# Kernel optimization log

Hardware: AMD Instinct MI355X
Metric: run time of the kernel (lower is better)

The kernel has to match this reference:

```python
import jax, jax.numpy as jnp
import numpy as np

B, LC, LP = 8, 1024, 512
D, H, F, V, NL = 512, 8, 2048, 70, 4
MAXLEN = 2048
HD = D // H
EPS = 1e-5


def setup_inputs() -> dict:
    key = jax.random.key(0)
    ks = iter(jax.random.split(key, 64))
    s = lambda *sh: jax.random.normal(next(ks), sh, jnp.float32) * 0.02
    inp = {}
    inp['cds'] = jax.random.randint(next(ks), (B, LC), 0, V)
    inp['enc_prot'] = jax.random.normal(next(ks), (B, LP, D), jnp.float32)
    causal = jnp.tril(jnp.ones((LC, LC), jnp.int32))
    inp['cds_mask'] = jnp.broadcast_to(causal[None, None], (B, 1, LC, LC))
    inp['prot_mask'] = jnp.ones((B, 1, 1, LP), jnp.int32)
    inp['tok_emb'] = s(V, D)
    inp['pos_emb'] = s(MAXLEN, D)
    for p in ['sa', 'ca']:
        for m in ['q', 'k', 'v', 'o']:
            inp[f'{p}_w{m}'] = s(NL, D, D)
            inp[f'{p}_b{m}'] = jnp.zeros((NL, D), jnp.float32)
    inp['ff_w1'] = s(NL, D, F)
    inp['ff_b1'] = jnp.zeros((NL, F), jnp.float32)
    inp['ff_w2'] = s(NL, F, D)
    inp['ff_b2'] = jnp.zeros((NL, D), jnp.float32)
    for i in [1, 2, 3]:
        inp[f'ln{i}_g'] = jnp.ones((NL, D), jnp.float32)
        inp[f'ln{i}_b'] = jnp.zeros((NL, D), jnp.float32)
    inp['fc_out_w'] = s(D, V)
    inp['fc_out_b'] = jnp.zeros((V,), jnp.float32)
    return inp


def layernorm(x, g, b):
    mu = jnp.mean(x, -1, keepdims=True)
    var = jnp.var(x, -1, keepdims=True)
    return (x - mu) * jax.lax.rsqrt(var + EPS) * g + b


def mha(q_in, k_in, v_in, wq, bq, wk, bk, wv, bv, wo, bo, mask):
    b, lq, _ = q_in.shape
    lk = k_in.shape[1]
    q = (q_in @ wq + bq).reshape(b, lq, H, HD).transpose(0, 2, 1, 3)
    k = (k_in @ wk + bk).reshape(b, lk, H, HD).transpose(0, 2, 1, 3)
    v = (v_in @ wv + bv).reshape(b, lk, H, HD).transpose(0, 2, 1, 3)
    scores = jnp.einsum('bhqd,bhkd->bhqk', q, k) / jnp.sqrt(jnp.float32(HD))
    scores = jnp.where(mask == 0, -jnp.inf, scores)
    attn = jax.nn.softmax(scores, axis=-1)
    out = jnp.einsum('bhqk,bhkd->bhqd', attn, v)
    out = out.transpose(0, 2, 1, 3).reshape(b, lq, D)
    return out @ wo + bo, attn


def reference(cds, enc_prot, cds_mask, prot_mask, tok_emb, pos_emb,
              sa_wq, sa_bq, sa_wk, sa_bk, sa_wv, sa_bv, sa_wo, sa_bo,
              ca_wq, ca_bq, ca_wk, ca_bk, ca_wv, ca_bv, ca_wo, ca_bo,
              ff_w1, ff_b1, ff_w2, ff_b2,
              ln1_g, ln1_b, ln2_g, ln2_b, ln3_g, ln3_b,
              fc_out_w, fc_out_b):
    lc = cds.shape[1]
    x = tok_emb[cds] * jnp.sqrt(jnp.float32(D)) + pos_emb[:lc][None]
    attn = None
    for i in range(NL):
        sa, _ = mha(x, x, x, sa_wq[i], sa_bq[i], sa_wk[i], sa_bk[i],
                    sa_wv[i], sa_bv[i], sa_wo[i], sa_bo[i], cds_mask)
        x = layernorm(x + sa, ln1_g[i], ln1_b[i])
        ca, attn = mha(x, enc_prot, enc_prot, ca_wq[i], ca_bq[i], ca_wk[i], ca_bk[i],
                       ca_wv[i], ca_bv[i], ca_wo[i], ca_bo[i], prot_mask)
        x = layernorm(x + ca, ln2_g[i], ln2_b[i])
        ff = jax.nn.relu(x @ ff_w1[i] + ff_b1[i]) @ ff_w2[i] + ff_b2[i]
        x = layernorm(x + ff, ln3_g[i], ln3_b[i])
    logits = x @ fc_out_w + fc_out_b
    return logits, attn
```

## Files before the change

### kernel.cpp

```cpp
#include <hip/hip_runtime.h>

typedef __attribute__((ext_vector_type(8))) short bf16x8;
typedef __attribute__((ext_vector_type(4))) short bf16x4;
typedef __attribute__((ext_vector_type(2))) short bf16x2;
typedef __attribute__((ext_vector_type(4))) float f32x4;

#define D_MODEL 512
#define N_HEADS 8
#define HEAD_DIM 64
#define SEQ_C 1024
#define SEQ_P 512
#define BATCH 8
#define FFDIM 2048
#define VOCAB 70
#define NLAYER 4
#define MQ (BATCH*SEQ_C)
#define MKV (BATCH*SEQ_P)
#define KSTR 72

__device__ __forceinline__ short f2bs(float f) {
  union { float f; unsigned u; } v; v.f = f;
  unsigned r = (v.u + 0x7FFFu + ((v.u >> 16) & 1u)) >> 16;
  return (short)r;
}

__device__ __forceinline__ void gl_lds16(const void* g, void* l) {
  __builtin_amdgcn_global_load_lds(
      (const __attribute__((address_space(1))) void*)g,
      (__attribute__((address_space(3))) void*)l, 16, 0, 0);
}

__global__ __launch_bounds__(256)
void embed_kernel(const int* __restrict__ cds, const float* __restrict__ tok,
                  const float* __restrict__ pos, float* __restrict__ x,
                  short* __restrict__ xb) {
  int idx = blockIdx.x * 256 + threadIdx.x;
  int row = idx >> 9, c = idx & 511;
  int l = row & (SEQ_C - 1);
  int t = cds[row];
  float v = tok[t * D_MODEL + c] * 22.627416997969522f + pos[l * D_MODEL + c];
  x[idx] = v;
  xb[idx] = f2bs(v);
}

__global__ __launch_bounds__(256)
void cvtf2b_kernel(const float* __restrict__ in, short* __restrict__ out) {
  int i = (blockIdx.x * 256 + threadIdx.x) * 4;
  float4 v = *(const float4*)(in + i);
  bf16x4 o;
  o[0] = f2bs(v.x); o[1] = f2bs(v.y); o[2] = f2bs(v.z); o[3] = f2bs(v.w);
  *(bf16x4*)(out + i) = o;
}

struct WtArgs {
  const float* src[8];
  short* dst[8];
  size_t ldz[8];
  int row_off[8];
};

__global__ __launch_bounds__(256)
void wtrans8_kernel(WtArgs a) {
  __shared__ float T[32][33];
  int z = blockIdx.z;
  int job = z >> 2, layer = z & 3;
  const float* W = a.src[job] + (size_t)layer * D_MODEL * D_MODEL;
  short* Wt = a.dst[job] + (size_t)layer * a.ldz[job];
  int row_off = a.row_off[job];
  int n0 = blockIdx.x * 32, k0 = blockIdx.y * 32;
  int r = threadIdx.x >> 3, c4 = (threadIdx.x & 7) * 4;
  float4 v = *(const float4*)(W + (size_t)(k0 + r) * D_MODEL + n0 + c4);
  T[c4 + 0][r] = v.x; T[c4 + 1][r] = v.y; T[c4 + 2][r] = v.z; T[c4 + 3][r] = v.w;
  __syncthreads();
  bf16x4 o;
  o[0] = f2bs(T[r][c4 + 0]); o[1] = f2bs(T[r][c4 + 1]);
  o[2] = f2bs(T[r][c4 + 2]); o[3] = f2bs(T[r][c4 + 3]);
  *(bf16x4*)&Wt[(size_t)(row_off + n0 + r) * D_MODEL + k0 + c4] = o;
}

__global__ __launch_bounds__(256)
void wtrans_kernel(const float* __restrict__ W, short* __restrict__ Wt,
                   int K, int N, size_t dst_ldz) {
  __shared__ float T[32][33];
  size_t lo_s = (size_t)blockIdx.z * K * N;
  size_t lo_d = (size_t)blockIdx.z * dst_ldz;
  int n0 = blockIdx.x * 32, k0 = blockIdx.y * 32;
  int r = threadIdx.x >> 3, c4 = (threadIdx.x & 7) * 4;
  float4 v = *(const float4*)(W + lo_s + (size_t)(k0 + r) * N + n0 + c4);
  T[c4 + 0][r] = v.x; T[c4 + 1][r] = v.y; T[c4 + 2][r] = v.z; T[c4 + 3][r] = v.w;
  __syncthreads();
  bf16x4 o;
  o[0] = f2bs(T[r][c4 + 0]); o[1] = f2bs(T[r][c4 + 1]);
  o[2] = f2bs(T[r][c4 + 2]); o[3] = f2bs(T[r][c4 + 3]);
  *(bf16x4*)&Wt[lo_d + (size_t)(n0 + r) * K + k0 + c4] = o;
}

__global__ __launch_bounds__(256)
void logits_wt_kernel(const float* __restrict__ w, short* __restrict__ wt) {
  int idx = blockIdx.x * 256 + threadIdx.x;
  int r = idx >> 9, c = idx & 511;
  wt[idx] = (r < VOCAB) ? f2bs(w[c * VOCAB + r]) : (short)0;
}

template<int ACT, int OMODE, int MT>
__global__ __launch_bounds__(256)
void gemm_mfma(const short* __restrict__ Ab, const short* __restrict__ Wt,
               const float* __restrict__ b0, const float* __restrict__ b1,
               const float* __restrict__ b2,
               float* __restrict__ Cf, short* __restrict__ Cb,
               int N, int K, int ldc, size_t segstride) {
  constexpr int MREP = MT / 32;
  __shared__ __align__(16) short As[2][MT * 32];
  __shared__ __align__(16) short Bs[2][4096];
  int tid = threadIdx.x, lane = tid & 63, w = tid >> 6;
  int quad = lane >> 4, ln = lane & 15;
  int row0 = blockIdx.x * MT, col0 = blockIdx.y * 128;
  int q0 = tid, q1 = tid + 256;
  const short* a0 = Ab + (size_t)(row0 + (q0 >> 2)) * K + (q0 & 3) * 8;
  const short* a1 = Ab + (size_t)(row0 + (q1 >> 2)) * K + (q1 & 3) * 8;
  const short* w0 = Wt + (size_t)(col0 + (q0 >> 2)) * K + (q0 & 3) * 8;
  const short* w1 = Wt + (size_t)(col0 + (q1 >> 2)) * K + (q1 & 3) * 8;
  int wr = (w >> 1) * (MT / 2), wc = (w & 1) * 64;
  f32x4 acc[MREP][4];
  #pragma unroll
  for (int mb = 0; mb < MREP; mb++)
    #pragma unroll
    for (int nb = 0; nb < 4; nb++) acc[mb][nb] = (f32x4){0.f, 0.f, 0.f, 0.f};

  int nt = K >> 5;
#define STG(ko, buf) do { \
    gl_lds16(a0 + (ko), &As[buf][w * 512]); \
    if (MT == 128) gl_lds16(a1 + (ko), &As[buf][MT * 16 + w * 512]); \
    gl_lds16(w0 + (ko), &Bs[buf][w * 512]); \
    gl_lds16(w1 + (ko), &Bs[buf][2048 + w * 512]); } while (0)

  STG(0, 0);
  __syncthreads();
  for (int t = 0; t < nt; t++) {
    int cur = t & 1;
    if (t + 1 < nt) STG((t + 1) << 5, cur ^ 1);
    bf16x8 af[MREP], bfr[4];
    #pragma unroll
    for (int i = 0; i < MREP; i++)
      af[i] = *(const bf16x8*)&As[cur][(wr + i * 16 + ln) * 32 + quad * 8];
    #pragma unroll
    for (int i = 0; i < 4; i++)
      bfr[i] = *(const bf16x8*)&Bs[cur][(wc + i * 16 + ln) * 32 + quad * 8];
    #pragma unroll
    for (int mb = 0; mb < MREP; mb++)
      #pragma unroll
      for (int nb = 0; nb < 4; nb++)
        acc[mb][nb] = __builtin_amdgcn_mfma_f32_16x16x32_bf16(
            af[mb], bfr[nb], acc[mb][nb], 0, 0, 0);
    __syncthreads();
  }
#undef STG

  int colb = col0 + wc;
  const float* bp = b0;
  if (OMODE == 2) {
    int seg = colb >> 9;
    bp = (seg == 0) ? b0 : (seg == 1) ? b1 : b2;
  }
  float bv[4];
  #pragma unroll
  for (int nb = 0; nb < 4; nb++) {
    int col = colb + nb * 16 + ln;
    if (OMODE == 3)      bv[nb] = (col < ldc) ? bp[col] : 0.f;
    else if (OMODE == 2) bv[nb] = bp[col & 511];
    else                 bv[nb] = bp[col];
  }
  size_t segoff = (OMODE == 2) ? (size_t)(colb >> 9) * segstride : 0;
  #pragma unroll
  for (int mb = 0; mb < MREP; mb++)
    #pragma unroll
    for (int i = 0; i < 4; i++) {
      size_t r = (size_t)(row0 + wr + mb * 16 + quad * 4 + i);
      #pragma unroll
      for (int nb = 0; nb < 4; nb++) {
        int col = colb + nb * 16 + ln;
        float v = acc[mb][nb][i] + bv[nb];
        if (ACT) v = fmaxf(v, 0.f);
        if (OMODE == 0)      Cf[r * ldc + col] = v;
        else if (OMODE == 1) Cb[r * ldc + col] = f2bs(v);
        else if (OMODE == 2) Cb[segoff + r * 512 + (col & 511)] = f2bs(v);
        else if (col < ldc)  Cf[r * ldc + col] = v;
      }
    }
}

template<bool CAUSAL, bool SAVE_ML>
__global__ __launch_bounds__(512)
void flash_mfma(const short* __restrict__ Q, const short* __restrict__ K,
                const short* __restrict__ V, short* __restrict__ O,
                float* __restrict__ m_out, float* __restrict__ l_out,
                int LQ, int LK) {
  __shared__ short Ks[2][64 * KSTR];
  __shared__ short Vt[2][64 * KSTR];
  __shared__ short Ps[8 * 16 * KSTR];
  const float scale = 0.125f;
  int qt = CAUSAL ? ((int)gridDim.x - 1 - (int)blockIdx.x) : (int)blockIdx.x;
  int bh = blockIdx.y;
  int b = bh >> 3, h = bh & 7;
  int tid = threadIdx.x, lane = tid & 63, w = tid >> 6;
  int quad = lane >> 4, ln = lane & 15;

  const short* qp = Q + (size_t)(b * LQ + qt * 128 + w * 16 + ln) * D_MODEL + h * HEAD_DIM;
  bf16x8 qf[2];
  qf[0] = *(const bf16x8*)(qp + quad * 8);
  qf[1] = *(const bf16x8*)(qp + 32 + quad * 8);

  int qrow = qt * 128 + w * 16 + ln;
  float m_q = -__builtin_inff(), l_q = 0.f;
  f32x4 o_acc[4];
  #pragma unroll
  for (int nb = 0; nb < 4; nb++) o_acc[nb] = (f32x4){0.f, 0.f, 0.f, 0.f};

  const short* Kb = K + (size_t)(b * LK) * D_MODEL + h * HEAD_DIM;
  const short* Vb = V + (size_t)(b * LK) * D_MODEL + h * HEAD_DIM;
  int sr = tid >> 3, sc = (tid & 7) * 8;
  int br4 = (tid >> 4) * 4, bc4 = (tid & 15) * 4;
  bool vst = tid < 256;

  bf16x8 kr;
  bf16x4 vr0, vr1, vr2, vr3;

#define LOADKV(KT) do { \
    kr = *(const bf16x8*)(Kb + (size_t)((KT) * 64 + sr) * D_MODEL + sc); \
    if (vst) { \
      const short* vg_ = Vb + (size_t)((KT) * 64 + br4) * D_MODEL + bc4; \
      vr0 = *(const bf16x4*)(vg_); \
      vr1 = *(const bf16x4*)(vg_ + D_MODEL); \
      vr2 = *(const bf16x4*)(vg_ + 2 * D_MODEL); \
      vr3 = *(const bf16x4*)(vg_ + 3 * D_MODEL); } } while (0)

#define STORKV(BUF) do { \
    *(bf16x8*)&Ks[BUF][sr * KSTR + sc] = kr; \
    if (vst) { \
      _Pragma("unroll") \
      for (int jj = 0; jj < 4; jj++) { \
        bf16x4 t_; \
        t_[0] = vr0[jj]; t_[1] = vr1[jj]; t_[2] = vr2[jj]; t_[3] = vr3[jj]; \
        *(bf16x4*)&Vt[BUF][(bc4 + jj) * KSTR + br4] = t_; } } } while (0)

  int nkt = CAUSAL ? (2 * qt + 2) : (LK >> 6);
  LOADKV(0);
  STORKV(0);
  if (nkt > 1) LOADKV(1);
  __syncthreads();

  for (int kt = 0; kt < nkt; kt++) {
    int cur = kt & 1;
    if (kt + 1 < nkt) {
      STORKV(cur ^ 1);
      if (kt + 2 < nkt) LOADKV(kt + 2);
    }

    f32x4 st[4];
    __builtin_amdgcn_s_setprio(1);
    #pragma unroll
    for (int nb = 0; nb < 4; nb++) {
      st[nb] = (f32x4){0.f, 0.f, 0.f, 0.f};
      bf16x8 kf0 = *(const bf16x8*)&Ks[cur][(nb * 16 + ln) * KSTR + quad * 8];
      bf16x8 kf1 = *(const bf16x8*)&Ks[cur][(nb * 16 + ln) * KSTR + 32 + quad * 8];
      st[nb] = __builtin_amdgcn_mfma_f32_16x16x32_bf16(kf0, qf[0], st[nb], 0, 0, 0);
      st[nb] = __builtin_amdgcn_mfma_f32_16x16x32_bf16(kf1, qf[1], st[nb], 0, 0, 0);
    }
    __builtin_amdgcn_s_setprio(0);

    float sv[4][4];
    float mt = -__builtin_inff();
    #pragma unroll
    for (int nb = 0; nb < 4; nb++)
      #pragma unroll
      for (int i = 0; i < 4; i++) {
        float v = st[nb][i] * scale;
        if (CAUSAL && (kt * 64 + nb * 16 + quad * 4 + i) > qrow) v = -__builtin_inff();
        sv[nb][i] = v;
        mt = fmaxf(mt, v);
      }
    mt = fmaxf(mt, __shfl_xor(mt, 16));
    mt = fmaxf(mt, __shfl_xor(mt, 32));
    float mnew = fmaxf(m_q, mt);
    float alpha = __expf(m_q - mnew);
    float rs = 0.f;
    bf16x4 pk[4];
    #pragma unroll
    for (int nb = 0; nb < 4; nb++)
      #pragma unroll
      for (int i = 0; i < 4; i++) {
        float p = __expf(sv[nb][i] - mnew);
        rs += p;
        pk[nb][i] = f2bs(p);
      }
    rs += __shfl_xor(rs, 16);
    rs += __shfl_xor(rs, 32);
    l_q = l_q * alpha + rs;
    m_q = mnew;

    #pragma unroll
    for (int nb = 0; nb < 4; nb++)
      *(bf16x4*)&Ps[w * 16 * KSTR + ln * KSTR + nb * 16 + quad * 4] = pk[nb];
    #pragma unroll
    for (int i = 0; i < 4; i++) {
      float ai = __shfl(alpha, ((lane >> 4) << 2) + i);
      #pragma unroll
      for (int nb = 0; nb < 4; nb++) o_acc[nb][i] *= ai;
    }

    __builtin_amdgcn_s_setprio(1);
    #pragma unroll
    for (int kb = 0; kb < 2; kb++) {
      bf16x8 pf = *(const bf16x8*)&Ps[w * 16 * KSTR + ln * KSTR + kb * 32 + quad * 8];
      #pragma unroll
      for (int nb = 0; nb < 4; nb++) {
        bf16x8 vf = *(const bf16x8*)&Vt[cur][(nb * 16 + ln) * KSTR + kb * 32 + quad * 8];
        o_acc[nb] = __builtin_amdgcn_mfma_f32_16x16x32_bf16(pf, vf, o_acc[nb], 0, 0, 0);
      }
    }
    __builtin_amdgcn_s_setprio(0);
    __syncthreads();
  }
#undef LOADKV
#undef STORKV

  short* Ob = O + (size_t)(b * LQ + qt * 128 + w * 16 + quad * 4) * D_MODEL + h * HEAD_DIM;
  #pragma unroll
  for (int i = 0; i < 4; i++) {
    float li = __shfl(l_q, ((lane >> 4) << 2) + i);
    float inv = 1.f / li;
    #pragma unroll
    for (int nb = 0; nb < 4; nb++)
      Ob[(size_t)i * D_MODEL + nb * 16 + ln] = f2bs(o_acc[nb][i] * inv);
  }
  if (SAVE_ML && lane < 16) {
    int r = bh * LQ + qt * 128 + w * 16 + lane;
    m_out[r] = m_q;
    l_out[r] = l_q;
  }
}

__global__ __launch_bounds__(256)
void attn_prob_mfma(const short* __restrict__ Q, const short* __restrict__ K,
                    const float* __restrict__ m_in, const float* __restrict__ l_in,
                    float* __restrict__ out) {
  __shared__ short Ks[64 * KSTR];
  const float scale = 0.125f;
  int qt = blockIdx.x, bh = blockIdx.y;
  int b = bh >> 3, h = bh & 7;
  int tid = threadIdx.x, lane = tid & 63, w = tid >> 6;
  int quad = lane >> 4, ln = lane & 15;
  const short* qp = Q + (size_t)(b * SEQ_C + qt * 64 + w * 16 + ln) * D_MODEL + h * HEAD_DIM;
  bf16x8 qf[2];
  qf[0] = *(const bf16x8*)(qp + quad * 8);
  qf[1] = *(const bf16x8*)(qp + 32 + quad * 8);
  float m_r[4], il[4];
  #pragma unroll
  for (int i = 0; i < 4; i++) {
    int r = bh * SEQ_C + qt * 64 + w * 16 + quad * 4 + i;
    m_r[i] = m_in[r]; il[i] = 1.f / l_in[r];
  }
  const short* Kb = K + (size_t)(b * SEQ_P) * D_MODEL + h * HEAD_DIM;
  int sr = tid >> 2, sc = (tid & 3) * 16;
  bf16x8 krA, krB;
  {
    const short* kg = Kb + (size_t)sr * D_MODEL + sc;
    krA = *(const bf16x8*)kg; krB = *(const bf16x8*)(kg + 8);
  }
  for (int kt = 0; kt < (SEQ_P >> 6); kt++) {
    __syncthreads();
    *(bf16x8*)&Ks[sr * KSTR + sc]     = krA;
    *(bf16x8*)&Ks[sr * KSTR + sc + 8] = krB;
    if (kt + 1 < (SEQ_P >> 6)) {
      const short* kg = Kb + (size_t)((kt + 1) * 64 + sr) * D_MODEL + sc;
      krA = *(const bf16x8*)kg; krB = *(const bf16x8*)(kg + 8);
    }
    __syncthreads();
    #pragma unroll
    for (int nb = 0; nb < 4; nb++) {
      f32x4 s = (f32x4){0.f, 0.f, 0.f, 0.f};
      bf16x8 kf0 = *(const bf16x8*)&Ks[(nb * 16 + ln) * KSTR + quad * 8];
      bf16x8 kf1 = *(const bf16x8*)&Ks[(nb * 16 + ln) * KSTR + 32 + quad * 8];
      s = __builtin_amdgcn_mfma_f32_16x16x32_bf16(qf[0], kf0, s, 0, 0, 0);
      s = __builtin_amdgcn_mfma_f32_16x16x32_bf16(qf[1], kf1, s, 0, 0, 0);
      #pragma unroll
      for (int i = 0; i < 4; i++) {
        size_t off = ((size_t)bh * SEQ_C + qt * 64 + w * 16 + quad * 4 + i) * SEQ_P
                   + kt * 64 + nb * 16 + ln;
        out[off] = __expf(s[i] * scale - m_r[i]) * il[i];
      }
    }
  }
}

__global__ __launch_bounds__(256)
void add_ln_kernel(float* __restrict__ x, const float* __restrict__ y,
                   const float* __restrict__ g, const float* __restrict__ b,
                   short* __restrict__ xb) {
  int row = blockIdx.x * 4 + (threadIdx.x >> 6);
  int lane = threadIdx.x & 63;
  float2* xr = (float2*)(x + (size_t)row * D_MODEL);
  bf16x2* xbr = (bf16x2*)(xb + (size_t)row * D_MODEL);
  const float2* yr = (const float2*)(y + (size_t)row * D_MODEL);
  float2 v[4]; float s = 0.f, sq = 0.f;
  #pragma unroll
  for (int i = 0; i < 4; i++) {
    int c = lane + 64 * i;
    float2 a = xr[c], d = yr[c];
    a.x += d.x; a.y += d.y;
    v[i] = a; s += a.x + a.y; sq += a.x * a.x + a.y * a.y;
  }
  #pragma unroll
  for (int m = 1; m < 64; m <<= 1) { s += __shfl_xor(s, m); sq += __shfl_xor(sq, m); }
  float mu = s * (1.0f / 512.0f);
  float var = sq * (1.0f / 512.0f) - mu * mu;
  float rstd = rsqrtf(var + 1e-5f);
  #pragma unroll
  for (int i = 0; i < 4; i++) {
    int c = lane + 64 * i;
    float r0 = (v[i].x - mu) * rstd * g[2 * c] + b[2 * c];
    float r1 = (v[i].y - mu) * rstd * g[2 * c + 1] + b[2 * c + 1];
    xr[c] = make_float2(r0, r1);
    bf16x2 o; o[0] = f2bs(r0); o[1] = f2bs(r1);
    xbr[c] = o;
  }
}

extern "C" void kernel_launch(void* const* d_in, const int* in_sizes, int n_in,
                              void* d_out, int out_size, void* d_ws, size_t ws_size,
                              hipStream_t stream) {
  (void)in_sizes; (void)n_in; (void)out_size; (void)ws_size;
  const int*   cds      = (const int*)d_in[0];
  const float* enc_prot = (const float*)d_in[1];
  const float* tok_emb  = (const float*)d_in[4];
  const float* pos_emb  = (const float*)d_in[5];
  const float* sa_wq = (const float*)d_in[6];  const float* sa_bq = (const float*)d_in[7];
  const float* sa_wk = (const float*)d_in[8];  const float* sa_bk = (const float*)d_in[9];
  const float* sa_wv = (const float*)d_in[10]; const float* sa_bv = (const float*)d_in[11];
  const float* sa_wo = (const float*)d_in[12]; const float* sa_bo = (const float*)d_in[13];
  const float* ca_wq = (const float*)d_in[14]; const float* ca_bq = (const float*)d_in[15];
  const float* ca_wk = (const float*)d_in[16]; const float* ca_bk = (const float*)d_in[17];
  const float* ca_wv = (const float*)d_in[18]; const float* ca_bv = (const float*)d_in[19];
  const float* ca_wo = (const float*)d_in[20]; const float* ca_bo = (const float*)d_in[21];
  const float* ff_w1 = (const float*)d_in[22]; const float* ff_b1 = (const float*)d_in[23];
  const float* ff_w2 = (const float*)d_in[24]; const float* ff_b2 = (const float*)d_in[25];
  const float* ln1_g = (const float*)d_in[26]; const float* ln1_b = (const float*)d_in[27];
  const float* ln2_g = (const float*)d_in[28]; const float* ln2_b = (const float*)d_in[29];
  const float* ln3_g = (const float*)d_in[30]; const float* ln3_b = (const float*)d_in[31];
  const float* fcw   = (const float*)d_in[32]; const float* fcb   = (const float*)d_in[33];

  float* x    = (float*)d_ws;
  float* y    = x + (size_t)MQ * D_MODEL;
  float* mbuf = y + (size_t)MQ * D_MODEL;
  float* lbuf = mbuf + (size_t)BATCH * N_HEADS * SEQ_C;
  short* xb   = (short*)(lbuf + (size_t)BATCH * N_HEADS * SEQ_C);
  short* qb   = xb + (size_t)MQ * D_MODEL;
  short* kb   = qb + (size_t)MQ * D_MODEL;
  short* vb   = kb + (size_t)MQ * D_MODEL;
  short* ctxb = vb + (size_t)MQ * D_MODEL;
  short* hb   = qb;
  short* encb = ctxb + (size_t)MQ * D_MODEL;
  short* wtb  = encb + (size_t)MKV * D_MODEL;
  short* wts  = wtb + (size_t)128 * D_MODEL;
  const size_t WSZ = (size_t)NLAYER * D_MODEL * D_MODEL;
  short* w_saqkv = wts;
  short* w_sao   = w_saqkv + 3 * WSZ;
  short* w_caq   = w_sao + WSZ;
  short* w_cakv  = w_caq + WSZ;
  short* w_cao   = w_cakv + 2 * WSZ;
  short* w_ff1   = w_cao + WSZ;
  short* w_ff2   = w_ff1 + (size_t)NLAYER * D_MODEL * FFDIM;

  float* logits = (float*)d_out;
  float* attn   = logits + (size_t)MQ * VOCAB;

  const size_t SEG = (size_t)MQ * D_MODEL;
  const size_t L1536 = (size_t)1536 * 512, L1024 = (size_t)1024 * 512, L512 = (size_t)512 * 512;

  embed_kernel<<<MQ * D_MODEL / 256, 256, 0, stream>>>(cds, tok_emb, pos_emb, x, xb);
  cvtf2b_kernel<<<(size_t)MKV * D_MODEL / 1024, 256, 0, stream>>>(enc_prot, encb);
  logits_wt_kernel<<<128 * D_MODEL / 256, 256, 0, stream>>>(fcw, wtb);
  {
    WtArgs a;
    a.src[0] = sa_wq; a.dst[0] = w_saqkv; a.ldz[0] = L1536; a.row_off[0] = 0;
    a.src[1] = sa_wk; a.dst[1] = w_saqkv; a.ldz[1] = L1536; a.row_off[1] = 512;
    a.src[2] = sa_wv; a.dst[2] = w_saqkv; a.ldz[2] = L1536; a.row_off[2] = 1024;
    a.src[3] = sa_wo; a.dst[3] = w_sao;   a.ldz[3] = L512;  a.row_off[3] = 0;
    a.src[4] = ca_wq; a.dst[4] = w_caq;   a.ldz[4] = L512;  a.row_off[4] = 0;
    a.src[5] = ca_wk; a.dst[5] = w_cakv;  a.ldz[5] = L1024; a.row_off[5] = 0;
    a.src[6] = ca_wv; a.dst[6] = w_cakv;  a.ldz[6] = L1024; a.row_off[6] = 512;
    a.src[7] = ca_wo; a.dst[7] = w_cao;   a.ldz[7] = L512;  a.row_off[7] = 0;
    wtrans8_kernel<<<dim3(16, 16, 8 * NLAYER), 256, 0, stream>>>(a);
  }
  wtrans_kernel<<<dim3(FFDIM / 32, D_MODEL / 32, NLAYER), 256, 0, stream>>>(
      ff_w1, w_ff1, D_MODEL, FFDIM, (size_t)FFDIM * 512);
  wtrans_kernel<<<dim3(D_MODEL / 32, FFDIM / 32, NLAYER), 256, 0, stream>>>(
      ff_w2, w_ff2, FFDIM, D_MODEL, (size_t)512 * FFDIM);

  dim3 gqkv(MQ / 128, 1536 / 128);
  dim3 gq64(MQ / 64, D_MODEL / 128);
  dim3 gkv64(MKV / 64, 1024 / 128);
  dim3 gf1(MQ / 128, FFDIM / 128);
  dim3 glg(MQ / 64, 1);
  dim3 ga(SEQ_C / 128, BATCH * N_HEADS);
  dim3 gap(SEQ_C / 64, BATCH * N_HEADS);

  for (int i = 0; i < NLAYER; i++) {
    size_t wo_ = (size_t)i * D_MODEL * D_MODEL, bo_ = (size_t)i * D_MODEL;
    size_t wf_ = (size_t)i * D_MODEL * FFDIM;
    gemm_mfma<0,2,128><<<gqkv, 256, 0, stream>>>(xb, w_saqkv + (size_t)i * L1536,
        sa_bq + bo_, sa_bk + bo_, sa_bv + bo_, nullptr, qb, 1536, 512, 512, SEG);
    flash_mfma<true,  false><<<ga, 512, 0, stream>>>(qb, kb, vb, ctxb, nullptr, nullptr, SEQ_C, SEQ_C);
    gemm_mfma<0,0,64><<<gq64, 256, 0, stream>>>(ctxb, w_sao + wo_,
        sa_bo + bo_, nullptr, nullptr, y, nullptr, 512, 512, 512, 0);
    add_ln_kernel<<<MQ / 4, 256, 0, stream>>>(x, y, ln1_g + bo_, ln1_b + bo_, xb);
    gemm_mfma<0,1,64><<<gq64, 256, 0, stream>>>(xb, w_caq + wo_,
        ca_bq + bo_, nullptr, nullptr, nullptr, qb, 512, 512, 512, 0);
    gemm_mfma<0,2,64><<<gkv64, 256, 0, stream>>>(encb, w_cakv + (size_t)i * L1024,
        ca_bk + bo_, ca_bv + bo_, nullptr, nullptr, kb, 1024, 512, 512, SEG);
    if (i == NLAYER - 1) {
      flash_mfma<false, true><<<ga, 512, 0, stream>>>(qb, kb, vb, ctxb, mbuf, lbuf, SEQ_C, SEQ_P);
      attn_prob_mfma<<<gap, 256, 0, stream>>>(qb, kb, mbuf, lbuf, attn);
    } else {
      flash_mfma<false, false><<<ga, 512, 0, stream>>>(qb, kb, vb, ctxb, nullptr, nullptr, SEQ_C, SEQ_P);
    }
    gemm_mfma<0,0,64><<<gq64, 256, 0, stream>>>(ctxb, w_cao + wo_,
        ca_bo + bo_, nullptr, nullptr, y, nullptr, 512, 512, 512, 0);
    add_ln_kernel<<<MQ / 4, 256, 0, stream>>>(x, y, ln2_g + bo_, ln2_b + bo_, xb);
    gemm_mfma<1,1,128><<<gf1, 256, 0, stream>>>(xb, w_ff1 + wf_,
        ff_b1 + (size_t)i * FFDIM, nullptr, nullptr, nullptr, hb, FFDIM, 512, FFDIM, 0);
    gemm_mfma<0,0,64><<<gq64, 256, 0, stream>>>(hb, w_ff2 + wf_,
        ff_b2 + bo_, nullptr, nullptr, y, nullptr, 512, FFDIM, 512, 0);
    add_ln_kernel<<<MQ / 4, 256, 0, stream>>>(x, y, ln3_g + bo_, ln3_b + bo_, xb);
  }
  gemm_mfma<0,3,64><<<glg, 256, 0, stream>>>(xb, wtb,
      fcb, nullptr, nullptr, logits, nullptr, 128, 512, VOCAB, 0);
}
```

Before: 1.279 ms.

## Merge QKV and cross-KV GEMMs, split-K FF2, lazy softmax rescale with exp2

```diff
diff --git a/kernel.cpp b/kernel.cpp
--- a/kernel.cpp
+++ b/kernel.cpp
@@ -17,6 +17,7 @@
 #define MQ (BATCH*SEQ_C)
 #define MKV (BATCH*SEQ_P)
 #define KSTR 72
+#define SCALE2 0.18033688011112043f
 
 __device__ __forceinline__ short f2bs(float f) {
   union { float f; unsigned u; } v; v.f = f;
@@ -102,12 +103,13 @@
   wt[idx] = (r < VOCAB) ? f2bs(w[c * VOCAB + r]) : (short)0;
 }
 
-template<int ACT, int OMODE, int MT>
+template<int ACT, int OMODE, int MT, int KSPLIT = 0>
 __global__ __launch_bounds__(256)
 void gemm_mfma(const short* __restrict__ Ab, const short* __restrict__ Wt,
                const float* __restrict__ b0, const float* __restrict__ b1,
                const float* __restrict__ b2,
-               float* __restrict__ Cf, short* __restrict__ Cb,
+               float* __restrict__ Cf, float* __restrict__ Cf2,
+               short* __restrict__ Cb,
                int N, int K, int ldc, size_t segstride) {
   constexpr int MREP = MT / 32;
   __shared__ __align__(16) short As[2][MT * 32];
@@ -115,11 +117,14 @@
   int tid = threadIdx.x, lane = tid & 63, w = tid >> 6;
   int quad = lane >> 4, ln = lane & 15;
   int row0 = blockIdx.x * MT, col0 = blockIdx.y * 128;
+  int kz = KSPLIT ? (int)blockIdx.z : 0;
+  int Keff = KSPLIT ? (K >> 1) : K;
+  int koff = kz * Keff;
   int q0 = tid, q1 = tid + 256;
-  const short* a0 = Ab + (size_t)(row0 + (q0 >> 2)) * K + (q0 & 3) * 8;
-  const short* a1 = Ab + (size_t)(row0 + (q1 >> 2)) * K + (q1 & 3) * 8;
-  const short* w0 = Wt + (size_t)(col0 + (q0 >> 2)) * K + (q0 & 3) * 8;
-  const short* w1 = Wt + (size_t)(col0 + (q1 >> 2)) * K + (q1 & 3) * 8;
+  const short* a0 = Ab + (size_t)(row0 + (q0 >> 2)) * K + koff + (q0 & 3) * 8;
+  const short* a1 = Ab + (size_t)(row0 + (q1 >> 2)) * K + koff + (q1 & 3) * 8;
+  const short* w0 = Wt + (size_t)(col0 + (q0 >> 2)) * K + koff + (q0 & 3) * 8;
+  const short* w1 = Wt + (size_t)(col0 + (q1 >> 2)) * K + koff + (q1 & 3) * 8;
   int wr = (w >> 1) * (MT / 2), wc = (w & 1) * 64;
   f32x4 acc[MREP][4];
   #pragma unroll
@@ -127,7 +132,7 @@
     #pragma unroll
     for (int nb = 0; nb < 4; nb++) acc[mb][nb] = (f32x4){0.f, 0.f, 0.f, 0.f};
 
-  int nt = K >> 5;
+  int nt = Keff >> 5;
 #define STG(ko, buf) do { \
     gl_lds16(a0 + (ko), &As[buf][w * 512]); \
     if (MT == 128) gl_lds16(a1 + (ko), &As[buf][MT * 16 + w * 512]); \
@@ -166,10 +171,12 @@
   #pragma unroll
   for (int nb = 0; nb < 4; nb++) {
     int col = colb + nb * 16 + ln;
-    if (OMODE == 3)      bv[nb] = (col < ldc) ? bp[col] : 0.f;
+    if (KSPLIT && kz)    bv[nb] = 0.f;
+    else if (OMODE == 3) bv[nb] = (col < ldc) ? bp[col] : 0.f;
     else if (OMODE == 2) bv[nb] = bp[col & 511];
     else                 bv[nb] = bp[col];
   }
+  float* Co = (KSPLIT && kz) ? Cf2 : Cf;
   size_t segoff = (OMODE == 2) ? (size_t)(colb >> 9) * segstride : 0;
   #pragma unroll
   for (int mb = 0; mb < MREP; mb++)
@@ -181,10 +188,88 @@
         int col = colb + nb * 16 + ln;
         float v = acc[mb][nb][i] + bv[nb];
         if (ACT) v = fmaxf(v, 0.f);
-        if (OMODE == 0)      Cf[r * ldc + col] = v;
+        if (OMODE == 0)      Co[r * ldc + col] = v;
         else if (OMODE == 1) Cb[r * ldc + col] = f2bs(v);
         else if (OMODE == 2) Cb[segoff + r * 512 + (col & 511)] = f2bs(v);
-        else if (col < ldc)  Cf[r * ldc + col] = v;
+        else if (col < ldc)  Co[r * ldc + col] = v;
+      }
+    }
+}
+
+__global__ __launch_bounds__(256)
+void gemm_mega(const short* __restrict__ A0, const short* __restrict__ W0,
+               const float* __restrict__ bq, const float* __restrict__ bk,
+               const float* __restrict__ bv0, short* __restrict__ out0,
+               const short* __restrict__ A1, const short* __restrict__ W1,
+               const float* __restrict__ bk2, const float* __restrict__ bv2,
+               short* __restrict__ out1) {
+  __shared__ __align__(16) short As[2][4096];
+  __shared__ __align__(16) short Bs[2][4096];
+  const int K = 512;
+  int bid = blockIdx.x;
+  int job = bid >= 768;
+  const short* Ab; const short* Wt; int row0, col0;
+  if (!job) { Ab = A0; Wt = W0; row0 = (bid & 63) << 7; col0 = (bid >> 6) << 7; }
+  else { int b2 = bid - 768; Ab = A1; Wt = W1; row0 = (b2 & 31) << 7; col0 = (b2 >> 5) << 7; }
+  int tid = threadIdx.x, lane = tid & 63, w = tid >> 6;
+  int quad = lane >> 4, ln = lane & 15;
+  int q0 = tid, q1 = tid + 256;
+  const short* a0 = Ab + (size_t)(row0 + (q0 >> 2)) * K + (q0 & 3) * 8;
+  const short* a1 = Ab + (size_t)(row0 + (q1 >> 2)) * K + (q1 & 3) * 8;
+  const short* w0 = Wt + (size_t)(col0 + (q0 >> 2)) * K + (q0 & 3) * 8;
+  const short* w1 = Wt + (size_t)(col0 + (q1 >> 2)) * K + (q1 & 3) * 8;
+  int wr = (w >> 1) * 64, wc = (w & 1) * 64;
+  f32x4 acc[4][4];
+  #pragma unroll
+  for (int mb = 0; mb < 4; mb++)
+    #pragma unroll
+    for (int nb = 0; nb < 4; nb++) acc[mb][nb] = (f32x4){0.f, 0.f, 0.f, 0.f};
+
+#define STG(ko, buf) do { \
+    gl_lds16(a0 + (ko), &As[buf][w * 512]); \
+    gl_lds16(a1 + (ko), &As[buf][2048 + w * 512]); \
+    gl_lds16(w0 + (ko), &Bs[buf][w * 512]); \
+    gl_lds16(w1 + (ko), &Bs[buf][2048 + w * 512]); } while (0)
+
+  STG(0, 0);
+  __syncthreads();
+  for (int t = 0; t < 16; t++) {
+    int cur = t & 1;
+    if (t + 1 < 16) STG((t + 1) << 5, cur ^ 1);
+    bf16x8 af[4], bfr[4];
+    #pragma unroll
+    for (int i = 0; i < 4; i++) {
+      af[i]  = *(const bf16x8*)&As[cur][(wr + i * 16 + ln) * 32 + quad * 8];
+      bfr[i] = *(const bf16x8*)&Bs[cur][(wc + i * 16 + ln) * 32 + quad * 8];
+    }
+    #pragma unroll
+    for (int mb = 0; mb < 4; mb++)
+      #pragma unroll
+      for (int nb = 0; nb < 4; nb++)
+        acc[mb][nb] = __builtin_amdgcn_mfma_f32_16x16x32_bf16(
+            af[mb], bfr[nb], acc[mb][nb], 0, 0, 0);
+    __syncthreads();
+  }
+#undef STG
+
+  int colb = col0 + wc;
+  int seg = colb >> 9;
+  const float* bp = job ? (seg ? bv2 : bk2)
+                        : (seg == 0 ? bq : seg == 1 ? bk : bv0);
+  short* ob = job ? (out1 + (size_t)seg * ((size_t)MKV * D_MODEL))
+                  : (out0 + (size_t)seg * ((size_t)MQ * D_MODEL));
+  float bvv[4];
+  #pragma unroll
+  for (int nb = 0; nb < 4; nb++) bvv[nb] = bp[(colb + nb * 16 + ln) & 511];
+  #pragma unroll
+  for (int mb = 0; mb < 4; mb++)
+    #pragma unroll
+    for (int i = 0; i < 4; i++) {
+      size_t r = (size_t)(row0 + wr + mb * 16 + quad * 4 + i);
+      #pragma unroll
+      for (int nb = 0; nb < 4; nb++) {
+        int col = colb + nb * 16 + ln;
+        ob[r * 512 + (col & 511)] = f2bs(acc[mb][nb][i] + bvv[nb]);
       }
     }
 }
@@ -198,7 +283,6 @@
   __shared__ short Ks[2][64 * KSTR];
   __shared__ short Vt[2][64 * KSTR];
   __shared__ short Ps[8 * 16 * KSTR];
-  const float scale = 0.125f;
   int qt = CAUSAL ? ((int)gridDim.x - 1 - (int)blockIdx.x) : (int)blockIdx.x;
   int bh = blockIdx.y;
   int b = bh >> 3, h = bh & 7;
@@ -270,42 +354,63 @@
 
     float sv[4][4];
     float mt = -__builtin_inff();
-    #pragma unroll
-    for (int nb = 0; nb < 4; nb++)
-      #pragma unroll
-      for (int i = 0; i < 4; i++) {
-        float v = st[nb][i] * scale;
-        if (CAUSAL && (kt * 64 + nb * 16 + quad * 4 + i) > qrow) v = -__builtin_inff();
-        sv[nb][i] = v;
-        mt = fmaxf(mt, v);
-      }
+    if (CAUSAL && (kt * 64 + 63 > qt * 128 + w * 16)) {
+      #pragma unroll
+      for (int nb = 0; nb < 4; nb++)
+        #pragma unroll
+        for (int i = 0; i < 4; i++) {
+          float v = st[nb][i] * SCALE2;
+          if ((kt * 64 + nb * 16 + quad * 4 + i) > qrow) v = -__builtin_inff();
+          sv[nb][i] = v;
+          mt = fmaxf(mt, v);
+        }
+    } else {
+      #pragma unroll
+      for (int nb = 0; nb < 4; nb++)
+        #pragma unroll
+        for (int i = 0; i < 4; i++) {
+          float v = st[nb][i] * SCALE2;
+          sv[nb][i] = v;
+          mt = fmaxf(mt, v);
+        }
+    }
     mt = fmaxf(mt, __shfl_xor(mt, 16));
     mt = fmaxf(mt, __shfl_xor(mt, 32));
-    float mnew = fmaxf(m_q, mt);
-    float alpha = __expf(m_q - mnew);
+    bool skip = __all(mt <= m_q + 8.0f) != 0;
+    float mnew = skip ? m_q : fmaxf(m_q, mt);
+    if (!skip) {
+      float alpha = __builtin_amdgcn_exp2f(m_q - mnew);
+      l_q *= alpha;
+      #pragma unroll
+      for (int i = 0; i < 4; i++) {
+        float ai = __shfl(alpha, ((lane >> 4) << 2) + i);
+        #pragma unroll
+        for (int nb = 0; nb < 4; nb++) o_acc[nb][i] *= ai;
+      }
+    }
+    m_q = mnew;
+
     float rs = 0.f;
-    bf16x4 pk[4];
-    #pragma unroll
-    for (int nb = 0; nb < 4; nb++)
-      #pragma unroll
-      for (int i = 0; i < 4; i++) {
-        float p = __expf(sv[nb][i] - mnew);
-        rs += p;
-        pk[nb][i] = f2bs(p);
-      }
+    unsigned pu[4][2];
+    #pragma unroll
+    for (int nb = 0; nb < 4; nb++) {
+      float p0 = __builtin_amdgcn_exp2f(sv[nb][0] - mnew);
+      float p1 = __builtin_amdgcn_exp2f(sv[nb][1] - mnew);
+      float p2 = __builtin_amdgcn_exp2f(sv[nb][2] - mnew);
+      float p3 = __builtin_amdgcn_exp2f(sv[nb][3] - mnew);
+      rs += (p0 + p1) + (p2 + p3);
+      asm("v_cvt_pk_bf16_f32 %0, %1, %2" : "=v"(pu[nb][0]) : "v"(p0), "v"(p1));
+      asm("v_cvt_pk_bf16_f32 %0, %1, %2" : "=v"(pu[nb][1]) : "v"(p2), "v"(p3));
+    }
     rs += __shfl_xor(rs, 16);
     rs += __shfl_xor(rs, 32);
-    l_q = l_q * alpha + rs;
-    m_q = mnew;
-
-    #pragma unroll
-    for (int nb = 0; nb < 4; nb++)
-      *(bf16x4*)&Ps[w * 16 * KSTR + ln * KSTR + nb * 16 + quad * 4] = pk[nb];
-    #pragma unroll
-    for (int i = 0; i < 4; i++) {
-      float ai = __shfl(alpha, ((lane >> 4) << 2) + i);
-      #pragma unroll
-      for (int nb = 0; nb < 4; nb++) o_acc[nb][i] *= ai;
+    l_q += rs;
+
+    #pragma unroll
+    for (int nb = 0; nb < 4; nb++) {
+      union { unsigned u[2]; bf16x4 v; } uu;
+      uu.u[0] = pu[nb][0]; uu.u[1] = pu[nb][1];
+      *(bf16x4*)&Ps[w * 16 * KSTR + ln * KSTR + nb * 16 + quad * 4] = uu.v;
     }
 
     __builtin_amdgcn_s_setprio(1);
@@ -345,7 +450,6 @@
                     const float* __restrict__ m_in, const float* __restrict__ l_in,
                     float* __restrict__ out) {
   __shared__ short Ks[64 * KSTR];
-  const float scale = 0.125f;
   int qt = blockIdx.x, bh = blockIdx.y;
   int b = bh >> 3, h = bh & 7;
   int tid = threadIdx.x, lane = tid & 63, w = tid >> 6;
@@ -387,14 +491,16 @@
       for (int i = 0; i < 4; i++) {
         size_t off = ((size_t)bh * SEQ_C + qt * 64 + w * 16 + quad * 4 + i) * SEQ_P
                    + kt * 64 + nb * 16 + ln;
-        out[off] = __expf(s[i] * scale - m_r[i]) * il[i];
+        out[off] = __builtin_amdgcn_exp2f(s[i] * SCALE2 - m_r[i]) * il[i];
       }
     }
   }
 }
 
+template<int NY2>
 __global__ __launch_bounds__(256)
 void add_ln_kernel(float* __restrict__ x, const float* __restrict__ y,
+                   const float* __restrict__ y2,
                    const float* __restrict__ g, const float* __restrict__ b,
                    short* __restrict__ xb) {
   int row = blockIdx.x * 4 + (threadIdx.x >> 6);
@@ -402,12 +508,14 @@
   float2* xr = (float2*)(x + (size_t)row * D_MODEL);
   bf16x2* xbr = (bf16x2*)(xb + (size_t)row * D_MODEL);
   const float2* yr = (const float2*)(y + (size_t)row * D_MODEL);
+  const float2* y2r = NY2 ? (const float2*)(y2 + (size_t)row * D_MODEL) : nullptr;
   float2 v[4]; float s = 0.f, sq = 0.f;
   #pragma unroll
   for (int i = 0; i < 4; i++) {
     int c = lane + 64 * i;
     float2 a = xr[c], d = yr[c];
     a.x += d.x; a.y += d.y;
+    if (NY2) { float2 e = y2r[c]; a.x += e.x; a.y += e.y; }
     v[i] = a; s += a.x + a.y; sq += a.x * a.x + a.y * a.y;
   }
   #pragma unroll
@@ -460,7 +568,9 @@
   short* ctxb = vb + (size_t)MQ * D_MODEL;
   short* hb   = qb;
   short* encb = ctxb + (size_t)MQ * D_MODEL;
-  short* wtb  = encb + (size_t)MKV * D_MODEL;
+  short* ckb  = encb + (size_t)MKV * D_MODEL;
+  short* cvb  = ckb + (size_t)MKV * D_MODEL;
+  short* wtb  = cvb + (size_t)MKV * D_MODEL;
   short* wts  = wtb + (size_t)128 * D_MODEL;
   const size_t WSZ = (size_t)NLAYER * D_MODEL * D_MODEL;
   short* w_saqkv = wts;
@@ -470,11 +580,11 @@
   short* w_cao   = w_cakv + 2 * WSZ;
   short* w_ff1   = w_cao + WSZ;
   short* w_ff2   = w_ff1 + (size_t)NLAYER * D_MODEL * FFDIM;
+  float* y2   = (float*)(w_ff2 + (size_t)NLAYER * D_MODEL * FFDIM);
 
   float* logits = (float*)d_out;
   float* attn   = logits + (size_t)MQ * VOCAB;
 
-  const size_t SEG = (size_t)MQ * D_MODEL;
   const size_t L1536 = (size_t)1536 * 512, L1024 = (size_t)1024 * 512, L512 = (size_t)512 * 512;
 
   embed_kernel<<<MQ * D_MODEL / 256, 256, 0, stream>>>(cds, tok_emb, pos_emb, x, xb);
@@ -497,10 +607,9 @@
   wtrans_kernel<<<dim3(D_MODEL / 32, FFDIM / 32, NLAYER), 256, 0, stream>>>(
       ff_w2, w_ff2, FFDIM, D_MODEL, (size_t)512 * FFDIM);
 
-  dim3 gqkv(MQ / 128, 1536 / 128);
   dim3 gq64(MQ / 64, D_MODEL / 128);
-  dim3 gkv64(MKV / 64, 1024 / 128);
   dim3 gf1(MQ / 128, FFDIM / 128);
+  dim3 gff2(MQ / 128, D_MODEL / 128, 2);
   dim3 glg(MQ / 64, 1);
   dim3 ga(SEQ_C / 128, BATCH * N_HEADS);
   dim3 gap(SEQ_C / 64, BATCH * N_HEADS);
@@ -508,31 +617,30 @@
   for (int i = 0; i < NLAYER; i++) {
     size_t wo_ = (size_t)i * D_MODEL * D_MODEL, bo_ = (size_t)i * D_MODEL;
     size_t wf_ = (size_t)i * D_MODEL * FFDIM;
-    gemm_mfma<0,2,128><<<gqkv, 256, 0, stream>>>(xb, w_saqkv + (size_t)i * L1536,
-        sa_bq + bo_, sa_bk + bo_, sa_bv + bo_, nullptr, qb, 1536, 512, 512, SEG);
+    gemm_mega<<<dim3(1024), 256, 0, stream>>>(
+        xb, w_saqkv + (size_t)i * L1536, sa_bq + bo_, sa_bk + bo_, sa_bv + bo_, qb,
+        encb, w_cakv + (size_t)i * L1024, ca_bk + bo_, ca_bv + bo_, ckb);
     flash_mfma<true,  false><<<ga, 512, 0, stream>>>(qb, kb, vb, ctxb, nullptr, nullptr, SEQ_C, SEQ_C);
     gemm_mfma<0,0,64><<<gq64, 256, 0, stream>>>(ctxb, w_sao + wo_,
-        sa_bo + bo_, nullptr, nullptr, y, nullptr, 512, 512, 512, 0);
-    add_ln_kernel<<<MQ / 4, 256, 0, stream>>>(x, y, ln1_g + bo_, ln1_b + bo_, xb);
+        sa_bo + bo_, nullptr, nullptr, y, nullptr, nullptr, 512, 512, 512, 0);
+    add_ln_kernel<0><<<MQ / 4, 256, 0, stream>>>(x, y, nullptr, ln1_g + bo_, ln1_b + bo_, xb);
     gemm_mfma<0,1,64><<<gq64, 256, 0, stream>>>(xb, w_caq + wo_,
-        ca_bq + bo_, nullptr, nullptr, nullptr, qb, 512, 512, 512, 0);
-    gemm_mfma<0,2,64><<<gkv64, 256, 0, stream>>>(encb, w_cakv + (size_t)i * L1024,
-        ca_bk + bo_, ca_bv + bo_, nullptr, nullptr, kb, 1024, 512, 512, SEG);
+        ca_bq + bo_, nullptr, nullptr, nullptr, nullptr, qb, 512, 512, 512, 0);
     if (i == NLAYER - 1) {
-      flash_mfma<false, true><<<ga, 512, 0, stream>>>(qb, kb, vb, ctxb, mbuf, lbuf, SEQ_C, SEQ_P);
-      attn_prob_mfma<<<gap, 256, 0, stream>>>(qb, kb, mbuf, lbuf, attn);
+      flash_mfma<false, true><<<ga, 512, 0, stream>>>(qb, ckb, cvb, ctxb, mbuf, lbuf, SEQ_C, SEQ_P);
+      attn_prob_mfma<<<gap, 256, 0, stream>>>(qb, ckb, mbuf, lbuf, attn);
     } else {
-      flash_mfma<false, false><<<ga, 512, 0, stream>>>(qb, kb, vb, ctxb, nullptr, nullptr, SEQ_C, SEQ_P);
+      flash_mfma<false, false><<<ga, 512, 0, stream>>>(qb, ckb, cvb, ctxb, nullptr, nullptr, SEQ_C, SEQ_P);
     }
     gemm_mfma<0,0,64><<<gq64, 256, 0, stream>>>(ctxb, w_cao + wo_,
-        ca_bo + bo_, nullptr, nullptr, y, nullptr, 512, 512, 512, 0);
-    add_ln_kernel<<<MQ / 4, 256, 0, stream>>>(x, y, ln2_g + bo_, ln2_b + bo_, xb);
+        ca_bo + bo_, nullptr, nullptr, y, nullptr, nullptr, 512, 512, 512, 0);
+    add_ln_kernel<0><<<MQ / 4, 256, 0, stream>>>(x, y, nullptr, ln2_g + bo_, ln2_b + bo_, xb);
     gemm_mfma<1,1,128><<<gf1, 256, 0, stream>>>(xb, w_ff1 + wf_,
-        ff_b1 + (size_t)i * FFDIM, nullptr, nullptr, nullptr, hb, FFDIM, 512, FFDIM, 0);
-    gemm_mfma<0,0,64><<<gq64, 256, 0, stream>>>(hb, w_ff2 + wf_,
-        ff_b2 + bo_, nullptr, nullptr, y, nullptr, 512, FFDIM, 512, 0);
-    add_ln_kernel<<<MQ / 4, 256, 0, stream>>>(x, y, ln3_g + bo_, ln3_b + bo_, xb);
+        ff_b1 + (size_t)i * FFDIM, nullptr, nullptr, nullptr, nullptr, hb, FFDIM, 512, FFDIM, 0);
+    gemm_mfma<0,0,128,1><<<gff2, 256, 0, stream>>>(hb, w_ff2 + wf_,
+        ff_b2 + bo_, nullptr, nullptr, y, y2, nullptr, 512, FFDIM, 512, 0);
+    add_ln_kernel<1><<<MQ / 4, 256, 0, stream>>>(x, y, y2, ln3_g + bo_, ln3_b + bo_, xb);
   }
   gemm_mfma<0,3,64><<<glg, 256, 0, stream>>>(xb, wtb,
-      fcb, nullptr, nullptr, logits, nullptr, 128, 512, VOCAB, 0);
-}
+      fcb, nullptr, nullptr, logits, nullptr, nullptr, 128, 512, VOCAB, 0);
+}
```

Result: faster. 1.207 ms (-5.6%).
